# Performance work log

Measured on AMD Instinct MI355X. Metric: run time of the kernel, lower is better.

## Reference

```python
import math
import jax, jax.numpy as jnp
import numpy as np

N, C, H, W = 32, 128, 56, 56


def unfold3(x, axis, dil):
    """F.unfold with 3-tap kernel along `axis`, dilation `dil`, padding `dil`.
    Input (n,c,h,w) -> output (n,c,3,h,w); tap k takes offset (k-1)*dil."""
    pad_cfg = [(0, 0)] * 4
    pad_cfg[axis] = (dil, dil)
    xp = jnp.pad(x, pad_cfg)
    size = x.shape[axis]
    taps = [jax.lax.slice_in_dim(xp, k * dil, k * dil + size, axis=axis) for k in range(3)]
    return jnp.stack(taps, axis=2)


def setup_inputs() -> dict:
    key = jax.random.key(0)
    k0, k1, k2, k3, k4 = jax.random.split(key, 5)
    x = jax.random.normal(k0, (N, C, H, W), dtype=jnp.float32)
    # trunc_normal_(std=0.02) approximated by normal * 0.02
    p2 = jax.random.normal(k1, (1, 1, 3, 1, W), dtype=jnp.float32) * 0.02
    # 1x1 conv weight (out=C, in=3C), kaiming-ish scale
    p3 = jax.random.normal(k2, (C, 3 * C), dtype=jnp.float32) * (1.0 / math.sqrt(3 * C))
    p5 = jax.random.normal(k3, (1, 1, H, W), dtype=jnp.float32) * 0.02
    p10 = jax.random.normal(k4, (1, C, 3, H, W), dtype=jnp.float32) * 0.02
    return {"x": x, "p2": p2, "p3": p3, "p5": p5, "p10": p10}


def reference(x, p2, p3, p5, p10):
    n, c, h, w = x.shape
    # t_1: vertical 3-tap unfold, dilation 2 -> (n,c,3,h,w)
    t1 = unfold3(x, axis=2, dil=2)
    t2 = p2 * t1                                              # (n,c,3,h,w)
    # t_3: 1x1 conv over the c*3 channel view
    t3 = jnp.einsum('nkhw,ck->nchw', t1.reshape(n, c * 3, h, w), p3)
    # t_4: horizontal 3-tap unfold, dilation 1
    t4 = unfold3(t3, axis=3, dil=1)                           # (n,c,3,h,w)
    t5 = p5 * t3                                              # (n,c,h,w)
    # t_7/t_8: horizontal 3-tap unfold of x, dilation 2, softmax over taps
    t7 = unfold3(x, axis=3, dil=2)
    t8 = jax.nn.softmax(t7, axis=2)                           # (n,c,3,h,w)
    # t_9: bmm over spatial dim -> (n,c,c*3)
    t9 = jnp.einsum('ncx,ndx->ncd', x.reshape(n, c, h * w),
                    t4.reshape(n, c * 3, h * w)) / math.sqrt(h * w)
    t10 = p10 * t8                                            # (n,c,3,h,w)
    # t_11: memory-reinterpreting view: (n,1,c,h,w) - (n,3,c,h,w) -> back to (n,c,3,h,w)
    t11 = (t5[:, None] - t2.reshape(n, 3, c, h, w)).reshape(n, c, 3, h, w)
    t12 = t11 - t10                                           # (n,c,3,h,w)
    # t_13: bmm over c*3 -> (n,c,h*w)
    t13 = jnp.einsum('ncd,ndx->ncx', t9,
                     t12.reshape(n, c * 3, h * w)) / math.sqrt(c * 3)
    return t13.reshape(n, c, h, w)
```

## Files before the change

### kernel.cpp

```cpp
#include <hip/hip_runtime.h>
#include <stdint.h>

#define NB 32
#define C_ 128
#define H_ 56
#define W_ 56
#define HW 3136
#define KD 384

typedef __attribute__((ext_vector_type(8))) short bf16x8;
typedef __attribute__((ext_vector_type(4))) float f32x4;

__device__ inline uint16_t f2bf(float f) {
    uint32_t u = __float_as_uint(f);
    return (uint16_t)((u + 0x7FFFu + ((u >> 16) & 1u)) >> 16);
}
__device__ inline float bf2f(uint16_t b) {
    return __uint_as_float(((uint32_t)b) << 16);
}

__global__ __launch_bounds__(256) void p1_xtp(const float* __restrict__ x,
                                              uint16_t* __restrict__ xtp,
                                              uint16_t* __restrict__ xb) {
    __shared__ uint16_t lt[56][136];
    const int h = blockIdx.x, n = blockIdx.y, tid = threadIdx.x;
    const int c = tid >> 1, wh = tid & 1;
    const float* xr = &x[(((size_t)n * C_ + c) * H_ + h) * W_ + wh * 28];
    uint32_t pk[14];
#pragma unroll
    for (int q = 0; q < 7; ++q) {
        float4 v = *(const float4*)&xr[q * 4];
        int wb = wh * 28 + q * 4;
        uint16_t b0 = f2bf(v.x), b1 = f2bf(v.y), b2 = f2bf(v.z), b3 = f2bf(v.w);
        lt[wb + 0][c] = b0;
        lt[wb + 1][c] = b1;
        lt[wb + 2][c] = b2;
        lt[wb + 3][c] = b3;
        pk[q * 2]     = (uint32_t)b0 | ((uint32_t)b1 << 16);
        pk[q * 2 + 1] = (uint32_t)b2 | ((uint32_t)b3 << 16);
    }
    {
        uint16_t* xrow = &xb[(((size_t)n * C_ + c) * H_ + h) * 64 + wh * 28];
#pragma unroll
        for (int q = 0; q < 7; ++q)
            *(uint2*)&xrow[q * 4] = make_uint2(pk[q * 2], pk[q * 2 + 1]);
        if (wh == 1) {
            uint4 z = {0, 0, 0, 0};
            *(uint4*)&xrow[28] = z;
        }
    }
    __syncthreads();
    const int w = tid >> 2, qc = tid & 3;
    uint16_t* dst = &xtp[((((size_t)n * H_ + h) * 64 + w)) * C_ + qc * 32];
    if (w < 56) {
        const uint32_t* s = (const uint32_t*)&lt[w][qc * 32];
        uint4 a = *(const uint4*)(s);
        uint4 b = *(const uint4*)(s + 4);
        uint4 c4 = *(const uint4*)(s + 8);
        uint4 d4 = *(const uint4*)(s + 12);
        *(uint4*)dst = a;
        *(uint4*)(dst + 8) = b;
        *(uint4*)(dst + 16) = c4;
        *(uint4*)(dst + 24) = d4;
    } else {
        uint4 z = {0, 0, 0, 0};
        *(uint4*)dst = z;
        *(uint4*)(dst + 8) = z;
        *(uint4*)(dst + 16) = z;
        *(uint4*)(dst + 24) = z;
    }
}

__global__ __launch_bounds__(256) void p2_ap(const float* __restrict__ p3,
                                             uint16_t* __restrict__ ap) {
    int i = blockIdx.x * 256 + threadIdx.x;
    int c = i / KD, dp = i - c * KD;
    int tap = dp >> 7, c2 = dp & 127;
    ap[i] = f2bf(p3[c * KD + 3 * c2 + tap]);
}

__global__ __launch_bounds__(256) void k1(const uint16_t* __restrict__ xtp,
                                          const uint16_t* __restrict__ ap,
                                          uint16_t* __restrict__ t3b) {
    __shared__ uint16_t smem[3 * 64 * 128];
    const int h = blockIdx.x, n = blockIdx.y, tid = threadIdx.x;
    const int lane = tid & 63, wid = tid >> 6;
    const int wm = wid >> 1, wn = wid & 1;

    for (int t = tid; t < 3072; t += 256) {
        int tap = t >> 10, r = t & 1023, w = r >> 4, qp = r & 15;
        int q = qp ^ (w & 7);
        int hh = h + 2 * (tap - 1);
        uint4 v = {0, 0, 0, 0};
        if ((unsigned)hh < (unsigned)H_)
            v = *(const uint4*)&xtp[((((size_t)n * H_ + hh) * 64 + w)) * C_ + q * 8];
        *(uint4*)&smem[tap * 8192 + w * 128 + qp * 8] = v;
    }
    __syncthreads();

    f32x4 acc[4][2] = {};
    for (int ks = 0; ks < 12; ++ks) {
        int tap = ks >> 2, kk = ks & 3;
        bf16x8 a[4], b[2];
#pragma unroll
        for (int m = 0; m < 4; ++m) {
            int c = wm * 64 + m * 16 + (lane & 15);
            a[m] = *(const bf16x8*)&ap[c * KD + ks * 32 + (lane >> 4) * 8];
        }
#pragma unroll
        for (int nt = 0; nt < 2; ++nt) {
            int w = wn * 32 + nt * 16 + (lane & 15);
            int q = kk * 4 + (lane >> 4);
            b[nt] = *(const bf16x8*)&smem[tap * 8192 + w * 128 + (q ^ (w & 7)) * 8];
        }
#pragma unroll
        for (int m = 0; m < 4; ++m)
#pragma unroll
            for (int nt = 0; nt < 2; ++nt)
                acc[m][nt] = __builtin_amdgcn_mfma_f32_16x16x32_bf16(a[m], b[nt], acc[m][nt], 0, 0, 0);
    }
    __syncthreads();

    uint16_t* lrow = smem;
#pragma unroll
    for (int m = 0; m < 4; ++m)
#pragma unroll
        for (int nt = 0; nt < 2; ++nt)
#pragma unroll
            for (int r = 0; r < 4; ++r) {
                int c = wm * 64 + m * 16 + (lane >> 4) * 4 + r;
                int w = wn * 32 + nt * 16 + (lane & 15);
                lrow[c * 72 + w] = f2bf(acc[m][nt][r]);
            }
    __syncthreads();

    const uint32_t* lrowd = (const uint32_t*)smem;
    for (int t = tid; t < 1024; t += 256) {
        int c = t >> 3, ch = t & 7;
        int m0 = c * 36 + ch * 4;
        uint4 o = make_uint4(lrowd[m0], lrowd[m0 + 1], lrowd[m0 + 2], lrowd[m0 + 3]);
        *(uint4*)&t3b[(((size_t)n * C_ + c) * H_ + h) * 64 + ch * 8] = o;
    }
}

__global__ __launch_bounds__(512) void k2(const uint16_t* __restrict__ xb,
                                          const uint16_t* __restrict__ t3b,
                                          uint16_t* __restrict__ part16) {
    __shared__ uint16_t xs[128 * 64];
    __shared__ uint16_t ts[128 * 64];
    const int bx = blockIdx.x;
    const int hc = bx / 3, tap = bx - hc * 3;
    const int n = blockIdx.y;
    const int tid = threadIdx.x, lane = tid & 63, wid = tid >> 6;
    const int wm = wid >> 2, wn = wid & 3;

    f32x4 acc[4][2] = {};
    for (int hr = 0; hr < 8; ++hr) {
        const int h = hc * 8 + hr;
        __syncthreads();
        for (int t = tid; t < 1024; t += 512) {
            int c = t >> 3, qp = t & 7, q = qp ^ (c & 7);
            uint4 v = *(const uint4*)&xb[(((size_t)n * C_ + c) * H_ + h) * 64 + q * 8];
            *(uint4*)&xs[c * 64 + qp * 8] = v;
        }
        for (int t = tid; t < 1024; t += 512) {
            int c2 = t >> 3, qp = t & 7, q = qp ^ (c2 & 7);
            const uint16_t* row = &t3b[(((size_t)n * C_ + c2) * H_ + h) * 64];
            uint4 v = *(const uint4*)&row[q * 8];
            uint4 o;
            if (tap == 1) {
                o = v;
            } else if (tap == 2) {
                uint32_t nx = (q < 7) ? *(const uint32_t*)&row[q * 8 + 8] : 0u;
                o.x = (v.y << 16) | (v.x >> 16);
                o.y = (v.z << 16) | (v.y >> 16);
                o.z = (v.w << 16) | (v.z >> 16);
                o.w = (nx << 16)  | (v.w >> 16);
            } else {
                uint32_t pv = (q > 0) ? *(const uint32_t*)&row[q * 8 - 2] : 0u;
                o.x = (v.x << 16) | (pv >> 16);
                o.y = (v.y << 16) | (v.x >> 16);
                o.z = (v.z << 16) | (v.y >> 16);
                o.w = (v.w << 16) | (v.z >> 16);
            }
            *(uint4*)&ts[c2 * 64 + qp * 8] = o;
        }
        __syncthreads();
#pragma unroll
        for (int ks = 0; ks < 2; ++ks) {
            bf16x8 a[4], b[2];
#pragma unroll
            for (int m = 0; m < 4; ++m) {
                int c = wm * 64 + m * 16 + (lane & 15);
                int q = ks * 4 + (lane >> 4);
                a[m] = *(const bf16x8*)&xs[c * 64 + (q ^ (c & 7)) * 8];
            }
#pragma unroll
            for (int nt = 0; nt < 2; ++nt) {
                int c2 = wn * 32 + nt * 16 + (lane & 15);
                int q = ks * 4 + (lane >> 4);
                b[nt] = *(const bf16x8*)&ts[c2 * 64 + (q ^ (c2 & 7)) * 8];
            }
#pragma unroll
            for (int m = 0; m < 4; ++m)
#pragma unroll
                for (int nt = 0; nt < 2; ++nt)
                    acc[m][nt] = __builtin_amdgcn_mfma_f32_16x16x32_bf16(a[m], b[nt], acc[m][nt], 0, 0, 0);
        }
    }
#pragma unroll
    for (int m = 0; m < 4; ++m)
#pragma unroll
        for (int nt = 0; nt < 2; ++nt)
#pragma unroll
            for (int r = 0; r < 4; ++r) {
                int c = wm * 64 + m * 16 + (lane >> 4) * 4 + r;
                int col = wn * 32 + nt * 16 + (lane & 15);
                part16[((((size_t)bx * NB + n) * C_ + c) << 7) + col] = f2bf(acc[m][nt][r]);
            }
}

__global__ __launch_bounds__(256) void kr(const uint16_t* __restrict__ part16,
                                          uint16_t* __restrict__ acat) {
    int idx = blockIdx.x * 256 + threadIdx.x;
    int fl = idx * 4;
    int nc = fl / KD, dp = fl - nc * KD;
    int tap = dp >> 7, c2 = dp & 127;
    float s0 = 0.f, s1 = 0.f, s2 = 0.f, s3 = 0.f;
#pragma unroll
    for (int hc = 0; hc < 7; ++hc) {
        uint2 v = *(const uint2*)&part16[((((size_t)(hc * 3 + tap)) * NB * C_ + nc) << 7) + c2];
        s0 += bf2f((uint16_t)(v.x & 0xffff));
        s1 += bf2f((uint16_t)(v.x >> 16));
        s2 += bf2f((uint16_t)(v.y & 0xffff));
        s3 += bf2f((uint16_t)(v.y >> 16));
    }
    const float sc = 1.f / 56.f;
    uint2 o;
    o.x = (uint32_t)f2bf(s0 * sc) | ((uint32_t)f2bf(s1 * sc) << 16);
    o.y = (uint32_t)f2bf(s2 * sc) | ((uint32_t)f2bf(s3 * sc) << 16);
    *(uint2*)&acat[(size_t)nc * 512 + dp] = o;
}

__global__ __launch_bounds__(256) void ka2(uint16_t* __restrict__ acat) {
    int t = blockIdx.x * 256 + threadIdx.x;
    int nc = t >> 3, m0 = (t & 7) * 16;
    uint16_t* row = &acat[(size_t)nc * 512];
#pragma unroll
    for (int mi = 0; mi < 16; ++mi) {
        int m = m0 + mi;
        float s = 0.f;
#pragma unroll
        for (int r = 0; r < 3; ++r) {
            int d = m + 128 * r;
            int q3 = d / 3;
            int dp = (d - q3 * 3) * 128 + q3;
            s += bf2f(row[dp]);
        }
        row[384 + m] = f2bf(s);
    }
}

__global__ __launch_bounds__(256) void kt(const float* __restrict__ p10,
                                          uint16_t* __restrict__ p10t) {
    const int h = blockIdx.x, tid = threadIdx.x;
    for (int idx = tid; idx < 3072; idx += 256) {
        int w = idx & 63, ch = idx >> 6;
        int dp0 = ch * 8;
        uint32_t pk[4];
#pragma unroll
        for (int j = 0; j < 8; ++j) {
            int dp = dp0 + j;
            int tap = dp >> 7, c2 = dp & 127;
            int dor = 3 * c2 + tap;
            float v = (w < W_) ? p10[(size_t)dor * HW + h * W_ + w] : 0.f;
            uint16_t bb = f2bf(v);
            if (j & 1) pk[j >> 1] |= ((uint32_t)bb) << 16;
            else       pk[j >> 1] = bb;
        }
        *(uint4*)&p10t[((size_t)h * 64 + w) * KD + dp0] = *(const uint4*)pk;
    }
}

__global__ __launch_bounds__(256, 4) void k3(const uint16_t* __restrict__ xtp,
                                             const uint16_t* __restrict__ t3b,
                                             const uint16_t* __restrict__ acat,
                                             const uint16_t* __restrict__ p10t,
                                             const float* __restrict__ p2,
                                             const float* __restrict__ p5,
                                             float* __restrict__ out) {
    __shared__ uint16_t tsm[32 * 512];
    const int bx = blockIdx.x, n = blockIdx.y, tid = threadIdx.x;
    const int h = bx >> 1, wbase = (bx & 1) << 5;
    const int lane = tid & 63, wid = tid >> 6;

    {
        const int w = tid & 31, seg = tid >> 5;
        const int wg = wbase + w;
        const int wsw = w & 7;
        float p2v[3];
#pragma unroll
        for (int tap = 0; tap < 3; ++tap)
            p2v[tap] = (wg < W_) ? p2[tap * W_ + wg] : 0.f;
        const size_t xrow = ((size_t)n * H_ + h) * 64;
        const int wgm2 = (wg >= 2) ? wg - 2 : 0;
        const int wgp2 = (wg + 2 < 64) ? wg + 2 : 63;

#pragma unroll
        for (int s = 0; s < 2; ++s) {
            const int c2b = (seg + s * 8) * 8;
            bf16x8 xh_v = *(const bf16x8*)&xtp[(xrow + wg) * C_ + c2b];
            bf16x8 xm_v = *(const bf16x8*)&xtp[(xrow + wgm2) * C_ + c2b];
            bf16x8 xp_v = *(const bf16x8*)&xtp[(xrow + wgp2) * C_ + c2b];
            float sm[3][8];
#pragma unroll
            for (int j = 0; j < 8; ++j) {
                float a1 = bf2f((uint16_t)xh_v[j]);
                float a0 = (wg >= 2) ? bf2f((uint16_t)xm_v[j]) : 0.f;
                float a2 = bf2f((uint16_t)xp_v[j]);
                float mx = fmaxf(a0, fmaxf(a1, a2));
                float e0 = __expf(a0 - mx), e1 = __expf(a1 - mx), e2 = __expf(a2 - mx);
                float rs = 1.f / (e0 + e1 + e2);
                sm[0][j] = e0 * rs; sm[1][j] = e1 * rs; sm[2][j] = e2 * rs;
            }
#pragma unroll
            for (int tap = 0; tap < 3; ++tap) {
                bf16x8 xhh;
                float p2e;
                if (tap == 1) { xhh = xh_v; p2e = p2v[1]; }
                else {
                    const int hh = h + 2 * (tap - 1);
                    const bool hok = (unsigned)hh < (unsigned)H_;
                    const int hhc = hok ? hh : h;
                    xhh = *(const bf16x8*)&xtp[(((size_t)n * H_ + hhc) * 64 + wg) * C_ + c2b];
                    p2e = hok ? p2v[tap] : 0.f;
                }
                bf16x8 pv = *(const bf16x8*)&p10t[((size_t)h * 64 + wg) * KD + tap * 128 + c2b];
                uint32_t pk[4];
#pragma unroll
                for (int j = 0; j < 8; ++j) {
                    float val = -(p2e * bf2f((uint16_t)xhh[j]) + bf2f((uint16_t)pv[j]) * sm[tap][j]);
                    uint16_t bb = f2bf(val);
                    if (j & 1) pk[j >> 1] |= ((uint32_t)bb) << 16;
                    else       pk[j >> 1] = bb;
                }
                int q = (tap * 128 + c2b) >> 3;
                *(uint4*)&tsm[w * 512 + ((q ^ wsw) << 3)] = *(const uint4*)pk;
            }
        }
    }

    {
        const int c2f = tid >> 1;
        const int whl = (tid & 1) << 4;
        const uint16_t* t3r = &t3b[(((size_t)n * C_ + c2f) * H_ + h) * 64 + wbase + whl];
        const int qf = 48 + (c2f >> 3);
        const int cf7 = c2f & 7;
#pragma unroll
        for (int g = 0; g < 2; ++g) {
            bf16x8 tv = *(const bf16x8*)&t3r[g * 8];
#pragma unroll
            for (int j = 0; j < 8; ++j) {
                int wl = whl + g * 8 + j;
                int wwg = wbase + wl;
                float p5v = (wwg < W_) ? p5[h * W_ + wwg] : 0.f;
                tsm[wl * 512 + ((qf ^ (wl & 7)) << 3) + cf7] = f2bf(p5v * bf2f((uint16_t)tv[j]));
            }
        }
    }
    __syncthreads();

    const int wm = wid;
    f32x4 acc[2][2] = {};
    for (int ks = 0; ks < 16; ++ks) {
        bf16x8 a[2], b[2];
#pragma unroll
        for (int m = 0; m < 2; ++m) {
            int c = wm * 32 + m * 16 + (lane & 15);
            a[m] = *(const bf16x8*)&acat[((size_t)n * C_ + c) * 512 + ks * 32 + (lane >> 4) * 8];
        }
#pragma unroll
        for (int nt = 0; nt < 2; ++nt) {
            int wl = nt * 16 + (lane & 15);
            int q = ks * 4 + (lane >> 4);
            b[nt] = *(const bf16x8*)&tsm[wl * 512 + ((q ^ (wl & 7)) << 3)];
        }
#pragma unroll
        for (int m = 0; m < 2; ++m)
#pragma unroll
            for (int nt = 0; nt < 2; ++nt)
                acc[m][nt] = __builtin_amdgcn_mfma_f32_16x16x32_bf16(a[m], b[nt], acc[m][nt], 0, 0, 0);
    }

    const float s = 0.05103103630798287f;
#pragma unroll
    for (int m = 0; m < 2; ++m)
#pragma unroll
        for (int nt = 0; nt < 2; ++nt) {
            int wwg = wbase + nt * 16 + (lane & 15);
            if (wwg < W_) {
                int c = wm * 32 + m * 16 + (lane >> 4) * 4;
                float* dst = &out[(((size_t)n * C_ + c) * H_ + h) * W_ + wwg];
#pragma unroll
                for (int r = 0; r < 4; ++r) dst[(size_t)r * HW] = acc[m][nt][r] * s;
            }
        }
}

extern "C" void kernel_launch(void* const* d_in, const int* in_sizes, int n_in,
                              void* d_out, int out_size, void* d_ws, size_t ws_size,
                              hipStream_t stream) {
    const float* x   = (const float*)d_in[0];
    const float* p2  = (const float*)d_in[1];
    const float* p3  = (const float*)d_in[2];
    const float* p5  = (const float*)d_in[3];
    const float* p10 = (const float*)d_in[4];
    float* out = (float*)d_out;

    uint8_t* w8 = (uint8_t*)d_ws;
    uint16_t* t3b    = (uint16_t*)(w8);
    uint16_t* ap     = (uint16_t*)(w8 + 29360128);
    uint16_t* xtp    = (uint16_t*)(w8 + 29458432);
    uint16_t* xb     = (uint16_t*)(w8 + 58818560);
    uint16_t* part16 = (uint16_t*)(w8 + 88178688);
    uint16_t* p10t   = (uint16_t*)(w8 + 88178688);
    uint16_t* acat   = (uint16_t*)(w8 + 110198784);

    p1_xtp<<<dim3(H_, NB), 256, 0, stream>>>(x, xtp, xb);
    p2_ap<<<dim3(192), 256, 0, stream>>>(p3, ap);
    k1<<<dim3(H_, NB), 256, 0, stream>>>(xtp, ap, t3b);
    k2<<<dim3(21, NB), 512, 0, stream>>>(xb, t3b, part16);
    kr<<<dim3(1536), 256, 0, stream>>>(part16, acat);
    ka2<<<dim3(128), 256, 0, stream>>>(acat);
    kt<<<dim3(H_), 256, 0, stream>>>(p10, p10t);
    k3<<<dim3(112, NB), 256, 0, stream>>>(xtp, t3b, acat, p10t, p2, p5, out);
}
```

Measured before the change: 235.1 us.

## Split t12 elementwise prologue out of final GEMM kernel into separate pass

The softmax and p2/p10 elementwise construction of the t12 operand moves out of the final GEMM kernel into a separate kernel kb2. kb2 writes bf16 tiles to workspace, and k3g then loads them into swizzled shared memory. The work is split into two passes by h parity so the staging buffer fits in the workspace region previously used by xb. The intent is to remove the redundant per-w-half recomputation and lighten k3's prologue so the GEMM runs with fewer registers. The cost is extra global write/read traffic and four kernel launches instead of one.

```diff
diff --git a/kernel.cpp b/kernel.cpp
--- a/kernel.cpp
+++ b/kernel.cpp
@@ -282,72 +282,85 @@
     }
 }
 
-__global__ __launch_bounds__(256, 4) void k3(const uint16_t* __restrict__ xtp,
-                                             const uint16_t* __restrict__ t3b,
-                                             const uint16_t* __restrict__ acat,
-                                             const uint16_t* __restrict__ p10t,
-                                             const float* __restrict__ p2,
-                                             const float* __restrict__ p5,
-                                             float* __restrict__ out) {
+__global__ __launch_bounds__(512) void kb2(const uint16_t* __restrict__ xtp,
+                                           const uint16_t* __restrict__ p10t,
+                                           const float* __restrict__ p2,
+                                           uint16_t* __restrict__ t12b, int hpar) {
+    const int hb = blockIdx.x, n = blockIdx.y, tid = threadIdx.x;
+    const int h = hb * 2 + hpar;
+    const int w = tid & 63, seg = tid >> 6;
+    float p2v[3];
+#pragma unroll
+    for (int tap = 0; tap < 3; ++tap)
+        p2v[tap] = (w < W_) ? p2[tap * W_ + w] : 0.f;
+    const size_t xrow = ((size_t)n * H_ + h) * 64;
+    const int wgm2 = (w >= 2) ? w - 2 : 0;
+    const int wgp2 = (w + 2 < 64) ? w + 2 : 63;
+    uint16_t* tile = &t12b[((size_t)n * 28 + hb) * 24576];
+
+#pragma unroll
+    for (int s = 0; s < 2; ++s) {
+        const int c2b = (seg + s * 8) * 8;
+        bf16x8 xh_v = *(const bf16x8*)&xtp[(xrow + w) * C_ + c2b];
+        bf16x8 xm_v = *(const bf16x8*)&xtp[(xrow + wgm2) * C_ + c2b];
+        bf16x8 xp_v = *(const bf16x8*)&xtp[(xrow + wgp2) * C_ + c2b];
+        float sm[3][8];
+#pragma unroll
+        for (int j = 0; j < 8; ++j) {
+            float a1 = bf2f((uint16_t)xh_v[j]);
+            float a0 = (w >= 2) ? bf2f((uint16_t)xm_v[j]) : 0.f;
+            float a2 = bf2f((uint16_t)xp_v[j]);
+            float mx = fmaxf(a0, fmaxf(a1, a2));
+            float e0 = __expf(a0 - mx), e1 = __expf(a1 - mx), e2 = __expf(a2 - mx);
+            float rs = 1.f / (e0 + e1 + e2);
+            sm[0][j] = e0 * rs; sm[1][j] = e1 * rs; sm[2][j] = e2 * rs;
+        }
+#pragma unroll
+        for (int tap = 0; tap < 3; ++tap) {
+            bf16x8 xhh;
+            float p2e;
+            if (tap == 1) { xhh = xh_v; p2e = p2v[1]; }
+            else {
+                const int hh = h + 2 * (tap - 1);
+                const bool hok = (unsigned)hh < (unsigned)H_;
+                const int hhc = hok ? hh : h;
+                xhh = *(const bf16x8*)&xtp[(((size_t)n * H_ + hhc) * 64 + w) * C_ + c2b];
+                p2e = hok ? p2v[tap] : 0.f;
+            }
+            bf16x8 pv = *(const bf16x8*)&p10t[((size_t)h * 64 + w) * KD + tap * 128 + c2b];
+            uint32_t pk[4];
+#pragma unroll
+            for (int j = 0; j < 8; ++j) {
+                float val = -(p2e * bf2f((uint16_t)xhh[j]) + bf2f((uint16_t)pv[j]) * sm[tap][j]);
+                uint16_t bb = f2bf(val);
+                if (j & 1) pk[j >> 1] |= ((uint32_t)bb) << 16;
+                else       pk[j >> 1] = bb;
+            }
+            int ch = tap * 16 + seg + s * 8;
+            *(uint4*)&tile[ch * 512 + w * 8] = *(const uint4*)pk;
+        }
+    }
+}
+
+__global__ __launch_bounds__(256, 4) void k3g(const uint16_t* __restrict__ t12b,
+                                              const uint16_t* __restrict__ t3b,
+                                              const uint16_t* __restrict__ acat,
+                                              const float* __restrict__ p5,
+                                              float* __restrict__ out, int hpar) {
     __shared__ uint16_t tsm[32 * 512];
     const int bx = blockIdx.x, n = blockIdx.y, tid = threadIdx.x;
-    const int h = bx >> 1, wbase = (bx & 1) << 5;
+    const int hb = bx >> 1, wb = bx & 1;
+    const int h = hb * 2 + hpar;
+    const int wbase = wb << 5;
     const int lane = tid & 63, wid = tid >> 6;
 
-    {
-        const int w = tid & 31, seg = tid >> 5;
-        const int wg = wbase + w;
-        const int wsw = w & 7;
-        float p2v[3];
-#pragma unroll
-        for (int tap = 0; tap < 3; ++tap)
-            p2v[tap] = (wg < W_) ? p2[tap * W_ + wg] : 0.f;
-        const size_t xrow = ((size_t)n * H_ + h) * 64;
-        const int wgm2 = (wg >= 2) ? wg - 2 : 0;
-        const int wgp2 = (wg + 2 < 64) ? wg + 2 : 63;
-
-#pragma unroll
-        for (int s = 0; s < 2; ++s) {
-            const int c2b = (seg + s * 8) * 8;
-            bf16x8 xh_v = *(const bf16x8*)&xtp[(xrow + wg) * C_ + c2b];
-            bf16x8 xm_v = *(const bf16x8*)&xtp[(xrow + wgm2) * C_ + c2b];
-            bf16x8 xp_v = *(const bf16x8*)&xtp[(xrow + wgp2) * C_ + c2b];
-            float sm[3][8];
-#pragma unroll
-            for (int j = 0; j < 8; ++j) {
-                float a1 = bf2f((uint16_t)xh_v[j]);
-                float a0 = (wg >= 2) ? bf2f((uint16_t)xm_v[j]) : 0.f;
-                float a2 = bf2f((uint16_t)xp_v[j]);
-                float mx = fmaxf(a0, fmaxf(a1, a2));
-                float e0 = __expf(a0 - mx), e1 = __expf(a1 - mx), e2 = __expf(a2 - mx);
-                float rs = 1.f / (e0 + e1 + e2);
-                sm[0][j] = e0 * rs; sm[1][j] = e1 * rs; sm[2][j] = e2 * rs;
-            }
-#pragma unroll
-            for (int tap = 0; tap < 3; ++tap) {
-                bf16x8 xhh;
-                float p2e;
-                if (tap == 1) { xhh = xh_v; p2e = p2v[1]; }
-                else {
-                    const int hh = h + 2 * (tap - 1);
-                    const bool hok = (unsigned)hh < (unsigned)H_;
-                    const int hhc = hok ? hh : h;
-                    xhh = *(const bf16x8*)&xtp[(((size_t)n * H_ + hhc) * 64 + wg) * C_ + c2b];
-                    p2e = hok ? p2v[tap] : 0.f;
-                }
-                bf16x8 pv = *(const bf16x8*)&p10t[((size_t)h * 64 + wg) * KD + tap * 128 + c2b];
-                uint32_t pk[4];
-#pragma unroll
-                for (int j = 0; j < 8; ++j) {
-                    float val = -(p2e * bf2f((uint16_t)xhh[j]) + bf2f((uint16_t)pv[j]) * sm[tap][j]);
-                    uint16_t bb = f2bf(val);
-                    if (j & 1) pk[j >> 1] |= ((uint32_t)bb) << 16;
-                    else       pk[j >> 1] = bb;
-                }
-                int q = (tap * 128 + c2b) >> 3;
-                *(uint4*)&tsm[w * 512 + ((q ^ wsw) << 3)] = *(const uint4*)pk;
-            }
-        }
+    const uint16_t* tile = &t12b[((size_t)n * 28 + hb) * 24576];
+#pragma unroll
+    for (int r = 0; r < 6; ++r) {
+        int idx = r * 256 + tid;
+        int ch = idx >> 5, wl = idx & 31;
+        uint4 v = *(const uint4*)&tile[ch * 512 + (wbase + wl) * 8];
+        *(uint4*)&tsm[wl * 512 + ((ch ^ (wl & 7)) << 3)] = v;
     }
 
     {
@@ -423,7 +436,8 @@
     uint16_t* xtp    = (uint16_t*)(w8 + 29458432);
     uint16_t* xb     = (uint16_t*)(w8 + 58818560);
     uint16_t* part16 = (uint16_t*)(w8 + 88178688);
-    uint16_t* p10t   = (uint16_t*)(w8 + 88178688);
+    uint16_t* t12b   = (uint16_t*)(w8 + 58818560);
+    uint16_t* p10t   = (uint16_t*)(w8 + 102858752);
     uint16_t* acat   = (uint16_t*)(w8 + 110198784);
 
     p1_xtp<<<dim3(H_, NB), 256, 0, stream>>>(x, xtp, xb);
@@ -433,5 +447,8 @@
     kr<<<dim3(1536), 256, 0, stream>>>(part16, acat);
     ka2<<<dim3(128), 256, 0, stream>>>(acat);
     kt<<<dim3(H_), 256, 0, stream>>>(p10, p10t);
-    k3<<<dim3(112, NB), 256, 0, stream>>>(xtp, t3b, acat, p10t, p2, p5, out);
-}
+    kb2<<<dim3(28, NB), 512, 0, stream>>>(xtp, p10t, p2, t12b, 0);
+    k3g<<<dim3(56, NB), 256, 0, stream>>>(t12b, t3b, acat, p5, out, 0);
+    kb2<<<dim3(28, NB), 512, 0, stream>>>(xtp, p10t, p2, t12b, 1);
+    k3g<<<dim3(56, NB), 256, 0, stream>>>(t12b, t3b, acat, p5, out, 1);
+}
```

Measured after the change: 274.9 us. 16.9% more time.
